# Kernel optimization log

Measured on AMD Instinct MI355X. Metric: run time of the kernel, lower is better.

The kernel has to match this reference:

```python
import jax, jax.numpy as jnp
import numpy as np

EPS = 1e-12


def t5_layer_norm(x, w):
    # RMS norm without mean subtraction (T5 style)
    var = jnp.mean(x * x, axis=-1, keepdims=True)
    return w * (x * jax.lax.rsqrt(var + EPS))


def gether(h, a_simi, t_simi, adj):
    # h: [B,S,S,D]; a_simi/t_simi: [B,S]; adj: [B,S,S]
    diag = jnp.einsum('bssd->bsd', h)                 # h[b,l,l,:]
    h_adj = jnp.einsum('bld,blk->blkd', diag, adj)    # diag broadcast by adjacency
    h_y = h * t_simi[:, None, :, None]                # t_simi varies along axis 2
    h_x = h * a_simi[:, :, None, None]                # a_simi varies along axis 1
    h_left = jnp.pad(h_y, ((0, 0), (0, 0), (1, 0), (0, 0)))[:, :, :-1, :]
    h_right = jnp.pad(h_y, ((0, 0), (0, 0), (0, 1), (0, 0)))[:, :, 1:, :]
    h_up = jnp.pad(h_x, ((0, 0), (1, 0), (0, 0), (0, 0)))[:, :-1, :, :]
    h_down = jnp.pad(h_x, ((0, 0), (0, 1), (0, 0), (0, 0)))[:, 1:, :, :]
    return h + h_adj + h_left + h_right + h_up + h_down


def setup_inputs() -> dict:
    key = jax.random.key(0)
    ks = jax.random.split(key, 10)
    B, S, D_in, D_out = 8, 96, 768, 256
    table = jax.random.normal(ks[0], (B, S, S, D_in), dtype=jnp.float32)
    a_simi = jax.random.uniform(ks[1], (B, S), dtype=jnp.float32)
    t_simi = jax.random.uniform(ks[2], (B, S), dtype=jnp.float32)
    adj_matrix = jax.random.uniform(ks[3], (B, S, S), dtype=jnp.float32)
    s1 = 1.0 / np.sqrt(D_in)
    W1 = jax.random.uniform(ks[4], (D_in, D_in), jnp.float32, -s1, s1)
    b1 = jax.random.uniform(ks[5], (D_in,), jnp.float32, -s1, s1)
    g1 = jnp.ones((D_in,), jnp.float32)
    W2 = jax.random.uniform(ks[6], (D_in, D_out), jnp.float32, -s1, s1)
    b2 = jax.random.uniform(ks[7], (D_out,), jnp.float32, -s1, s1)
    g2 = jnp.ones((D_out,), jnp.float32)
    return {"table": table, "a_simi": a_simi, "t_simi": t_simi,
            "adj_matrix": adj_matrix, "W1": W1, "b1": b1, "g1": g1,
            "W2": W2, "b2": b2, "g2": g2}


def reference(table, a_simi, t_simi, adj_matrix, W1, b1, g1, W2, b2, g2):
    h0 = table
    h1 = gether(h0, a_simi, t_simi, adj_matrix)
    h1 = jax.nn.relu(t5_layer_norm((h1 + h0) @ W1 + b1, g1))
    h2 = gether(h1, a_simi, t_simi, adj_matrix)
    h2 = jax.nn.relu(t5_layer_norm((h2 + h1) @ W2 + b2, g2))
    return h2
```

## Files before the change

### kernel.cpp

```cpp
#include <hip/hip_runtime.h>

typedef __bf16 bf16;
typedef __bf16 bf16x4 __attribute__((ext_vector_type(4)));
typedef __bf16 bf16x8 __attribute__((ext_vector_type(8)));
typedef float f32x4 __attribute__((ext_vector_type(4)));
typedef float floatx4 __attribute__((ext_vector_type(4)));

#define S 96
#define DIN 768
#define DOUT 256
#define MROWS 73728

__device__ static inline void async16(const bf16* g, bf16* l) {
    __builtin_amdgcn_global_load_lds(
        (const __attribute__((address_space(1))) void*)g,
        (__attribute__((address_space(3))) void*)l,
        16, 0, 0);
}

__global__ __launch_bounds__(256) void k_gether1(
    const float* __restrict__ H, const float* __restrict__ Asim,
    const float* __restrict__ Tsim, const float* __restrict__ Adj,
    bf16* __restrict__ X)
{
    __shared__ float adjs[S];
    __shared__ float ts[S];
    __shared__ float diagf[DIN];
    int b = blockIdx.x / S, l = blockIdx.x % S;
    int tid = threadIdx.x;
    long row0 = (long)(b * S + l) * S;
    if (tid < S) {
        adjs[tid] = Adj[(b * S + l) * S + tid];
        ts[tid]   = Tsim[b * S + tid];
    }
    for (int i = tid; i < DIN / 4; i += 256)
        *(f32x4*)&diagf[i * 4] = *(const f32x4*)&H[(row0 + l) * DIN + i * 4];
    float a_up = (l > 0)     ? Asim[b * S + l - 1] : 0.f;
    float a_dn = (l < S - 1) ? Asim[b * S + l + 1] : 0.f;
    long du = (l > 0)     ? -(long)S * DIN : 0;
    long dd = (l < S - 1) ?  (long)S * DIN : 0;
    __syncthreads();

    int lane = tid & 63, wv = tid >> 6;
    int k0 = blockIdx.y * (S / 2);
    for (int k = k0 + wv; k < k0 + S / 2; k += 4) {
        float tl = (k > 0)     ? ts[k - 1] : 0.f;
        float tr = (k < S - 1) ? ts[k + 1] : 0.f;
        long  dl = (k > 0)     ? -(long)DIN : 0;
        long  dr = (k < S - 1) ?  (long)DIN : 0;
        float aj = adjs[k];
        const float* hrow = H + (row0 + k) * DIN;
        bf16* xrow = X + (row0 + k) * DIN;
#pragma unroll
        for (int c = 0; c < 3; ++c) {
            int col = (lane + c * 64) * 4;
            const float* hc = hrow + col;
            f32x4 vc = *(const f32x4*)hc;
            f32x4 vl = *(const f32x4*)(hc + dl);
            f32x4 vr = *(const f32x4*)(hc + dr);
            f32x4 vu = *(const f32x4*)(hc + du);
            f32x4 vd = *(const f32x4*)(hc + dd);
            bf16x4 o;
#pragma unroll
            for (int j = 0; j < 4; ++j) {
                float v = 2.f * vc[j] + aj * diagf[col + j]
                        + tl * vl[j] + tr * vr[j]
                        + a_up * vu[j] + a_dn * vd[j];
                o[j] = (bf16)v;
            }
            *(bf16x4*)&xrow[col] = o;
        }
    }
}

__global__ __launch_bounds__(256) void k_gether2(
    const bf16* __restrict__ Y, const float* __restrict__ INV,
    const float* __restrict__ G1, const float* __restrict__ Asim,
    const float* __restrict__ Tsim, const float* __restrict__ Adj,
    bf16* __restrict__ X)
{
    __shared__ float adjs[S];
    __shared__ float ts[S];
    __shared__ float diagf[DIN];
    __shared__ float g1s[DIN];
    int b = blockIdx.x / S, l = blockIdx.x % S;
    int tid = threadIdx.x;
    long row0 = (long)(b * S + l) * S;
    for (int i = tid; i < DIN; i += 256) g1s[i] = G1[i];
    __syncthreads();
    if (tid < S) {
        adjs[tid] = Adj[(b * S + l) * S + tid];
        ts[tid]   = Tsim[b * S + tid];
        float iv = INV[row0 + l];
        bf16x8 yv = *(const bf16x8*)&Y[(row0 + l) * DIN + tid * 8];
#pragma unroll
        for (int j = 0; j < 8; ++j) {
            float v = g1s[tid * 8 + j] * (float)yv[j] * iv;
            diagf[tid * 8 + j] = v > 0.f ? v : 0.f;
        }
    }
    float a_up = (l > 0)     ? Asim[b * S + l - 1] : 0.f;
    float a_dn = (l < S - 1) ? Asim[b * S + l + 1] : 0.f;
    long du = (l > 0)     ? -(long)S * DIN : 0;
    long dd = (l < S - 1) ?  (long)S * DIN : 0;
    int ou = (l > 0) ? -S : 0;
    int od = (l < S - 1) ? S : 0;
    __syncthreads();

    int lane = tid & 63, wv = tid >> 6;
    int k0 = blockIdx.y * (S / 2);
    for (int k = k0 + wv; k < k0 + S / 2; k += 4) {
        float tl = (k > 0)     ? ts[k - 1] : 0.f;
        float tr = (k < S - 1) ? ts[k + 1] : 0.f;
        int   ol = (k > 0)     ? -1 : 0;
        int   orr = (k < S - 1) ? 1 : 0;
        float aj = adjs[k];
        float ivc = INV[row0 + k];
        float ivl = INV[row0 + k + ol];
        float ivr = INV[row0 + k + orr];
        float ivu = INV[row0 + k + ou];
        float ivd = INV[row0 + k + od];
        const bf16* yrow = Y + (row0 + k) * DIN;
        bf16* xrow = X + (row0 + k) * DIN;
#pragma unroll
        for (int c = 0; c < 3; ++c) {
            int col = (lane + c * 64) * 4;
            const bf16* yc = yrow + col;
            bf16x4 vc = *(const bf16x4*)yc;
            bf16x4 vl = *(const bf16x4*)(yc + (long)ol * DIN);
            bf16x4 vr = *(const bf16x4*)(yc + (long)orr * DIN);
            bf16x4 vu = *(const bf16x4*)(yc + du);
            bf16x4 vd = *(const bf16x4*)(yc + dd);
            bf16x4 o;
#pragma unroll
            for (int j = 0; j < 4; ++j) {
                float g = g1s[col + j];
                float hc_ = g * (float)vc[j] * ivc; hc_ = hc_ > 0.f ? hc_ : 0.f;
                float hl_ = g * (float)vl[j] * ivl; hl_ = hl_ > 0.f ? hl_ : 0.f;
                float hr_ = g * (float)vr[j] * ivr; hr_ = hr_ > 0.f ? hr_ : 0.f;
                float hu_ = g * (float)vu[j] * ivu; hu_ = hu_ > 0.f ? hu_ : 0.f;
                float hd_ = g * (float)vd[j] * ivd; hd_ = hd_ > 0.f ? hd_ : 0.f;
                float v = 2.f * hc_ + aj * diagf[col + j]
                        + tl * hl_ + tr * hr_ + a_up * hu_ + a_dn * hd_;
                o[j] = (bf16)v;
            }
            *(bf16x4*)&xrow[col] = o;
        }
    }
}

__global__ __launch_bounds__(256) void k_gemm1(
    const bf16* __restrict__ Xm, const bf16* __restrict__ WT,
    const float* __restrict__ bias, bf16* __restrict__ Y,
    float* __restrict__ ssq)
{
    constexpr int K = 768, N = 768;
    __shared__ __align__(16) bf16 As[128 * 32];
    __shared__ __align__(16) bf16 Bs[128 * 32];
    int t = threadIdx.x;
    int colBase = blockIdx.x * 128;
    int rowBase = blockIdx.y * 128;
    int lane = t & 63, w = t >> 6;
    int quad = lane >> 4, l16 = lane & 15;
    int wr = w >> 1, wc = w & 1;

    floatx4 acc[4][4];
#pragma unroll
    for (int i = 0; i < 4; ++i)
#pragma unroll
        for (int j = 0; j < 4; ++j) acc[i][j] = (floatx4)0.f;

    int chunk = (t & 3) ^ ((t >> 3) & 3);
    const bf16* gA = Xm + (size_t)(rowBase + (t >> 2)) * K + chunk * 8;
    const bf16* gB = WT + (size_t)(colBase + (t >> 2)) * K + chunk * 8;
    bf16* ldsA = &As[t * 8];
    bf16* ldsB = &Bs[t * 8];

    for (int kk = 0; kk < K; kk += 32) {
        __syncthreads();
        async16(gA + kk, ldsA);
        async16(gA + kk + 64 * K, ldsA + 2048);
        async16(gB + kk, ldsB);
        async16(gB + kk + 64 * K, ldsB + 2048);
        __syncthreads();
        bf16x8 af[4], bfr[4];
#pragma unroll
        for (int i = 0; i < 4; ++i) {
            int ra = wr * 64 + i * 16 + l16;
            af[i] = *(const bf16x8*)&As[ra * 32 + (quad ^ ((ra >> 1) & 3)) * 8];
        }
#pragma unroll
        for (int j = 0; j < 4; ++j) {
            int rb = wc * 64 + j * 16 + l16;
            bfr[j] = *(const bf16x8*)&Bs[rb * 32 + (quad ^ ((rb >> 1) & 3)) * 8];
        }
#pragma unroll
        for (int i = 0; i < 4; ++i)
#pragma unroll
            for (int j = 0; j < 4; ++j)
                acc[i][j] = __builtin_amdgcn_mfma_f32_16x16x32_bf16(
                    af[i], bfr[j], acc[i][j], 0, 0, 0);
    }

    float bv[4];
#pragma unroll
    for (int j = 0; j < 4; ++j)
        bv[j] = bias[colBase + wc * 64 + j * 16 + l16];
#pragma unroll
    for (int i = 0; i < 4; ++i) {
#pragma unroll
        for (int r = 0; r < 4; ++r) {
            int row = rowBase + wr * 64 + i * 16 + quad * 4 + r;
            bf16* yp = Y + (size_t)row * N + colBase + wc * 64 + l16;
            float s = 0.f;
#pragma unroll
            for (int j = 0; j < 4; ++j) {
                float v = acc[i][j][r] + bv[j];
                s += v * v;
                yp[j * 16] = (bf16)v;
            }
            s += __shfl_xor(s, 1);
            s += __shfl_xor(s, 2);
            s += __shfl_xor(s, 4);
            s += __shfl_xor(s, 8);
            if (l16 == 0) atomicAdd(&ssq[row], s);
        }
    }
}

__global__ __launch_bounds__(256, 2) void k_gemm2f(
    const bf16* __restrict__ Xm, const bf16* __restrict__ WT,
    const float* __restrict__ bias, const float* __restrict__ G2,
    float* __restrict__ out)
{
    constexpr int K = 768, N = 256;
    __shared__ __align__(16) bf16 As[128 * 32];
    __shared__ __align__(16) bf16 Bs[256 * 32];
    __shared__ float ssqs[2][128];
    int t = threadIdx.x;
    int rowBase = blockIdx.x * 128;
    int lane = t & 63, w = t >> 6;
    int quad = lane >> 4, l16 = lane & 15;
    int wr = w >> 1, wc = w & 1;

    floatx4 acc[4][8];
#pragma unroll
    for (int i = 0; i < 4; ++i)
#pragma unroll
        for (int j = 0; j < 8; ++j) acc[i][j] = (floatx4)0.f;

    int chunk = (t & 3) ^ ((t >> 3) & 3);
    const bf16* gA = Xm + (size_t)(rowBase + (t >> 2)) * K + chunk * 8;
    const bf16* gB = WT + (size_t)(t >> 2) * K + chunk * 8;
    bf16* ldsA = &As[t * 8];
    bf16* ldsB = &Bs[t * 8];

    for (int kk = 0; kk < K; kk += 32) {
        __syncthreads();
        async16(gA + kk, ldsA);
        async16(gA + kk + 64 * K, ldsA + 2048);
        async16(gB + kk, ldsB);
        async16(gB + kk + 64 * K, ldsB + 2048);
        async16(gB + kk + 128 * K, ldsB + 4096);
        async16(gB + kk + 192 * K, ldsB + 6144);
        __syncthreads();
        bf16x8 af[4], bfr[8];
#pragma unroll
        for (int i = 0; i < 4; ++i) {
            int ra = wr * 64 + i * 16 + l16;
            af[i] = *(const bf16x8*)&As[ra * 32 + (quad ^ ((ra >> 1) & 3)) * 8];
        }
#pragma unroll
        for (int j = 0; j < 8; ++j) {
            int rb = wc * 128 + j * 16 + l16;
            bfr[j] = *(const bf16x8*)&Bs[rb * 32 + (quad ^ ((rb >> 1) & 3)) * 8];
        }
#pragma unroll
        for (int i = 0; i < 4; ++i)
#pragma unroll
            for (int j = 0; j < 8; ++j)
                acc[i][j] = __builtin_amdgcn_mfma_f32_16x16x32_bf16(
                    af[i], bfr[j], acc[i][j], 0, 0, 0);
    }

    float bv[8], gv[8];
#pragma unroll
    for (int j = 0; j < 8; ++j) {
        int col = wc * 128 + j * 16 + l16;
        bv[j] = bias[col];
        gv[j] = G2[col];
    }
#pragma unroll
    for (int i = 0; i < 4; ++i) {
#pragma unroll
        for (int r = 0; r < 4; ++r) {
            float s = 0.f;
#pragma unroll
            for (int j = 0; j < 8; ++j) {
                float v = acc[i][j][r] + bv[j];
                s += v * v;
            }
            s += __shfl_xor(s, 1);
            s += __shfl_xor(s, 2);
            s += __shfl_xor(s, 4);
            s += __shfl_xor(s, 8);
            if (l16 == 0)
                ssqs[wc][wr * 64 + i * 16 + quad * 4 + r] = s;
        }
    }
    __syncthreads();
#pragma unroll
    for (int i = 0; i < 4; ++i) {
#pragma unroll
        for (int r = 0; r < 4; ++r) {
            int lr = wr * 64 + i * 16 + quad * 4 + r;
            float inv = rsqrtf((ssqs[0][lr] + ssqs[1][lr]) * (1.f / N) + 1e-12f);
            float* op = out + (size_t)(rowBase + lr) * N + wc * 128 + l16;
#pragma unroll
            for (int j = 0; j < 8; ++j) {
                float v = (acc[i][j][r] + bv[j]) * gv[j] * inv;
                op[j * 16] = v > 0.f ? v : 0.f;
            }
        }
    }
}

__global__ __launch_bounds__(256) void k_invr(float* ssq, int n, float invD)
{
    int i = blockIdx.x * 256 + threadIdx.x;
    if (i < n) ssq[i] = rsqrtf(ssq[i] * invD + 1e-12f);
}

__global__ __launch_bounds__(256) void k_castT(
    const float* __restrict__ in, bf16* __restrict__ out, int R, int C)
{
    __shared__ float tile[32][33];
    int lx = threadIdx.x & 31, ly = threadIdx.x >> 5;
    int c0 = blockIdx.x * 32, r0 = blockIdx.y * 32;
#pragma unroll
    for (int k = 0; k < 4; ++k)
        tile[ly + 8 * k][lx] = in[(size_t)(r0 + ly + 8 * k) * C + c0 + lx];
    __syncthreads();
#pragma unroll
    for (int k = 0; k < 4; ++k)
        out[(size_t)(c0 + ly + 8 * k) * R + r0 + lx] = (bf16)tile[lx][ly + 8 * k];
}

extern "C" void kernel_launch(void* const* d_in, const int* in_sizes, int n_in,
                              void* d_out, int out_size, void* d_ws, size_t ws_size,
                              hipStream_t stream)
{
    const float* table = (const float*)d_in[0];
    const float* asim  = (const float*)d_in[1];
    const float* tsim  = (const float*)d_in[2];
    const float* adj   = (const float*)d_in[3];
    const float* W1    = (const float*)d_in[4];
    const float* b1    = (const float*)d_in[5];
    const float* g1    = (const float*)d_in[6];
    const float* W2    = (const float*)d_in[7];
    const float* b2    = (const float*)d_in[8];
    const float* g2    = (const float*)d_in[9];
    float* out = (float*)d_out;

    char* ws = (char*)d_ws;
    const size_t SZ_X = (size_t)MROWS * DIN * 2;
    bf16*  X    = (bf16*)ws;
    bf16*  Y1   = (bf16*)(ws + SZ_X);
    bf16*  W1T  = (bf16*)(ws + 2 * SZ_X);
    bf16*  W2T  = (bf16*)(ws + 2 * SZ_X + 1179648);
    float* ssq1 = (float*)(ws + 2 * SZ_X + 1179648 + 393216);

    hipMemsetAsync(ssq1, 0, (size_t)MROWS * 4, stream);
    k_castT<<<dim3(DIN / 32, DIN / 32), 256, 0, stream>>>(W1, W1T, DIN, DIN);
    k_castT<<<dim3(DOUT / 32, DIN / 32), 256, 0, stream>>>(W2, W2T, DIN, DOUT);

    k_gether1<<<dim3(8 * S, 2), 256, 0, stream>>>(table, asim, tsim, adj, X);
    k_gemm1<<<dim3(DIN / 128, MROWS / 128), 256, 0, stream>>>(X, W1T, b1, Y1, ssq1);
    k_invr<<<MROWS / 256, 256, 0, stream>>>(ssq1, MROWS, 1.f / DIN);
    k_gether2<<<dim3(8 * S, 2), 256, 0, stream>>>(Y1, ssq1, g1, asim, tsim, adj, X);
    k_gemm2f<<<MROWS / 128, 256, 0, stream>>>(X, W2T, b2, g2, out);
}
```

Baseline: 680.7 us.

## Double-buffer GEMM LDS tiles and remap workgroups across XCDs

Both GEMM kernels now use two LDS buffers, issuing the async global-to-LDS loads for the next K-slice before running the MFMAs on the current one, so there is one barrier per iteration instead of two. The gether kernels and gemm1 also permute the block index so consecutive workgroups (which the hardware spreads round-robin across the 8 XCDs) map to neighbouring tiles, aiming for better L2 locality. Doubling LDS raises per-block shared memory, which may lower occupancy, especially for gemm2f. The ordering also relies on the end-of-iteration barrier to cover completion of the async loads.

```diff
diff --git a/kernel.cpp b/kernel.cpp
--- a/kernel.cpp
+++ b/kernel.cpp
@@ -26,7 +26,9 @@
     __shared__ float adjs[S];
     __shared__ float ts[S];
     __shared__ float diagf[DIN];
-    int b = blockIdx.x / S, l = blockIdx.x % S;
+    int bx = blockIdx.x;
+    bx = (bx & 7) * (gridDim.x >> 3) + (bx >> 3);
+    int b = bx / S, l = bx % S;
     int tid = threadIdx.x;
     long row0 = (long)(b * S + l) * S;
     if (tid < S) {
@@ -83,7 +85,9 @@
     __shared__ float ts[S];
     __shared__ float diagf[DIN];
     __shared__ float g1s[DIN];
-    int b = blockIdx.x / S, l = blockIdx.x % S;
+    int bx = blockIdx.x;
+    bx = (bx & 7) * (gridDim.x >> 3) + (bx >> 3);
+    int b = bx / S, l = bx % S;
     int tid = threadIdx.x;
     long row0 = (long)(b * S + l) * S;
     for (int i = tid; i < DIN; i += 256) g1s[i] = G1[i];
@@ -155,11 +159,13 @@
     float* __restrict__ ssq)
 {
     constexpr int K = 768, N = 768;
-    __shared__ __align__(16) bf16 As[128 * 32];
-    __shared__ __align__(16) bf16 Bs[128 * 32];
+    __shared__ __align__(16) bf16 As[2][128 * 32];
+    __shared__ __align__(16) bf16 Bs[2][128 * 32];
     int t = threadIdx.x;
-    int colBase = blockIdx.x * 128;
-    int rowBase = blockIdx.y * 128;
+    int wg = blockIdx.x;
+    wg = (wg & 7) * (gridDim.x >> 3) + (wg >> 3);
+    int colBase = (wg % 6) * 128;
+    int rowBase = (wg / 6) * 128;
     int lane = t & 63, w = t >> 6;
     int quad = lane >> 4, l16 = lane & 15;
     int wr = w >> 1, wc = w & 1;
@@ -173,26 +179,30 @@
     int chunk = (t & 3) ^ ((t >> 3) & 3);
     const bf16* gA = Xm + (size_t)(rowBase + (t >> 2)) * K + chunk * 8;
     const bf16* gB = WT + (size_t)(colBase + (t >> 2)) * K + chunk * 8;
-    bf16* ldsA = &As[t * 8];
-    bf16* ldsB = &Bs[t * 8];
-
+    int l8 = t * 8;
+
+    auto stage = [&](int buf, int kk) {
+        async16(gA + kk, &As[buf][l8]);
+        async16(gA + kk + 64 * K, &As[buf][l8 + 2048]);
+        async16(gB + kk, &Bs[buf][l8]);
+        async16(gB + kk + 64 * K, &Bs[buf][l8 + 2048]);
+    };
+
+    stage(0, 0);
+    __syncthreads();
+    int cur = 0;
     for (int kk = 0; kk < K; kk += 32) {
-        __syncthreads();
-        async16(gA + kk, ldsA);
-        async16(gA + kk + 64 * K, ldsA + 2048);
-        async16(gB + kk, ldsB);
-        async16(gB + kk + 64 * K, ldsB + 2048);
-        __syncthreads();
+        if (kk + 32 < K) stage(cur ^ 1, kk + 32);
         bf16x8 af[4], bfr[4];
 #pragma unroll
         for (int i = 0; i < 4; ++i) {
             int ra = wr * 64 + i * 16 + l16;
-            af[i] = *(const bf16x8*)&As[ra * 32 + (quad ^ ((ra >> 1) & 3)) * 8];
+            af[i] = *(const bf16x8*)&As[cur][ra * 32 + (quad ^ ((ra >> 1) & 3)) * 8];
         }
 #pragma unroll
         for (int j = 0; j < 4; ++j) {
             int rb = wc * 64 + j * 16 + l16;
-            bfr[j] = *(const bf16x8*)&Bs[rb * 32 + (quad ^ ((rb >> 1) & 3)) * 8];
+            bfr[j] = *(const bf16x8*)&Bs[cur][rb * 32 + (quad ^ ((rb >> 1) & 3)) * 8];
         }
 #pragma unroll
         for (int i = 0; i < 4; ++i)
@@ -200,6 +210,8 @@
             for (int j = 0; j < 4; ++j)
                 acc[i][j] = __builtin_amdgcn_mfma_f32_16x16x32_bf16(
                     af[i], bfr[j], acc[i][j], 0, 0, 0);
+        __syncthreads();
+        cur ^= 1;
     }
 
     float bv[4];
@@ -234,8 +246,8 @@
     float* __restrict__ out)
 {
     constexpr int K = 768, N = 256;
-    __shared__ __align__(16) bf16 As[128 * 32];
-    __shared__ __align__(16) bf16 Bs[256 * 32];
+    __shared__ __align__(16) bf16 As[2][128 * 32];
+    __shared__ __align__(16) bf16 Bs[2][256 * 32];
     __shared__ float ssqs[2][128];
     int t = threadIdx.x;
     int rowBase = blockIdx.x * 128;
@@ -252,28 +264,32 @@
     int chunk = (t & 3) ^ ((t >> 3) & 3);
     const bf16* gA = Xm + (size_t)(rowBase + (t >> 2)) * K + chunk * 8;
     const bf16* gB = WT + (size_t)(t >> 2) * K + chunk * 8;
-    bf16* ldsA = &As[t * 8];
-    bf16* ldsB = &Bs[t * 8];
-
+    int l8 = t * 8;
+
+    auto stage = [&](int buf, int kk) {
+        async16(gA + kk, &As[buf][l8]);
+        async16(gA + kk + 64 * K, &As[buf][l8 + 2048]);
+        async16(gB + kk, &Bs[buf][l8]);
+        async16(gB + kk + 64 * K, &Bs[buf][l8 + 2048]);
+        async16(gB + kk + 128 * K, &Bs[buf][l8 + 4096]);
+        async16(gB + kk + 192 * K, &Bs[buf][l8 + 6144]);
+    };
+
+    stage(0, 0);
+    __syncthreads();
+    int cur = 0;
     for (int kk = 0; kk < K; kk += 32) {
-        __syncthreads();
-        async16(gA + kk, ldsA);
-        async16(gA + kk + 64 * K, ldsA + 2048);
-        async16(gB + kk, ldsB);
-        async16(gB + kk + 64 * K, ldsB + 2048);
-        async16(gB + kk + 128 * K, ldsB + 4096);
-        async16(gB + kk + 192 * K, ldsB + 6144);
-        __syncthreads();
+        if (kk + 32 < K) stage(cur ^ 1, kk + 32);
         bf16x8 af[4], bfr[8];
 #pragma unroll
         for (int i = 0; i < 4; ++i) {
             int ra = wr * 64 + i * 16 + l16;
-            af[i] = *(const bf16x8*)&As[ra * 32 + (quad ^ ((ra >> 1) & 3)) * 8];
+            af[i] = *(const bf16x8*)&As[cur][ra * 32 + (quad ^ ((ra >> 1) & 3)) * 8];
         }
 #pragma unroll
         for (int j = 0; j < 8; ++j) {
             int rb = wc * 128 + j * 16 + l16;
-            bfr[j] = *(const bf16x8*)&Bs[rb * 32 + (quad ^ ((rb >> 1) & 3)) * 8];
+            bfr[j] = *(const bf16x8*)&Bs[cur][rb * 32 + (quad ^ ((rb >> 1) & 3)) * 8];
         }
 #pragma unroll
         for (int i = 0; i < 4; ++i)
@@ -281,6 +297,8 @@
             for (int j = 0; j < 8; ++j)
                 acc[i][j] = __builtin_amdgcn_mfma_f32_16x16x32_bf16(
                     af[i], bfr[j], acc[i][j], 0, 0, 0);
+        __syncthreads();
+        cur ^= 1;
     }
 
     float bv[8], gv[8];
@@ -375,7 +393,7 @@
     k_castT<<<dim3(DOUT / 32, DIN / 32), 256, 0, stream>>>(W2, W2T, DIN, DOUT);
 
     k_gether1<<<dim3(8 * S, 2), 256, 0, stream>>>(table, asim, tsim, adj, X);
-    k_gemm1<<<dim3(DIN / 128, MROWS / 128), 256, 0, stream>>>(X, W1T, b1, Y1, ssq1);
+    k_gemm1<<<dim3((DIN / 128) * (MROWS / 128)), 256, 0, stream>>>(X, W1T, b1, Y1, ssq1);
     k_invr<<<MROWS / 256, 256, 0, stream>>>(ssq1, MROWS, 1.f / DIN);
     k_gether2<<<dim3(8 * S, 2), 256, 0, stream>>>(Y1, ssq1, g1, asim, tsim, adj, X);
     k_gemm2f<<<MROWS / 128, 256, 0, stream>>>(X, W2T, b2, g2, out);
```

After: 642.1 us. -5.7%, faster.
